# Optimization experiments

Measured on AMD Instinct MI355X. Metric: run time of the kernel, lower is better.

Reference implementation:

```python
import jax, jax.numpy as jnp
import numpy as np
import math

B, LQ, S, D = 8, 4096, 77, 1024
H, HD = 16, 64
R, ALPHA = 192, 16.0
LORA_SCALE = ALPHA / R
N_SUBJ = 32


def setup_inputs() -> dict:
    key = jax.random.key(0)
    ks = jax.random.split(key, 16)
    w = 0.02
    return {
        "hidden_states": jax.random.normal(ks[0], (B, LQ, D), jnp.float32),
        "encoder_hidden_states": jax.random.normal(ks[1], (B, S, D), jnp.float32),
        "Wq": jax.random.normal(ks[2], (D, D), jnp.float32) * w,
        "Wk": jax.random.normal(ks[3], (D, D), jnp.float32) * w,
        "Wv": jax.random.normal(ks[4], (D, D), jnp.float32) * w,
        "Wo": jax.random.normal(ks[5], (D, D), jnp.float32) * w,
        "bo": jnp.zeros((D,), jnp.float32),
        "Ak": jax.random.normal(ks[6], (R, D), jnp.float32) * w,
        "Bk": jax.random.normal(ks[7], (D, R), jnp.float32) * w,
        "Av": jax.random.normal(ks[8], (R, D), jnp.float32) * w,
        "Bv": jax.random.normal(ks[9], (D, R), jnp.float32) * w,
        "Ao": jax.random.normal(ks[10], (R, D), jnp.float32) * w,
        "Bo": jax.random.normal(ks[11], (D, R), jnp.float32) * w,
        "cross_attn_scale_factor": jnp.ones((), jnp.float32),
        "subj_b": jax.random.randint(ks[12], (N_SUBJ,), 0, B, jnp.int32),
        "subj_n": jax.random.randint(ks[13], (N_SUBJ,), 0, S, jnp.int32),
    }


def _lora(x, A, Bm):
    # peft LoRA delta: scale * (x @ A^T) @ B^T
    return LORA_SCALE * ((x @ A.T) @ Bm.T)


def reference(hidden_states, encoder_hidden_states, Wq, Wk, Wv, Wo, bo,
              Ak, Bk, Av, Bv, Ao, Bo, cross_attn_scale_factor, subj_b, subj_n):
    hs, ehs = hidden_states, encoder_hidden_states
    # q_lora_updates_query=False -> query uses the base projection only
    q = hs @ Wq.T                                  # [B, LQ, D]
    k = ehs @ Wk.T + _lora(ehs, Ak, Bk)            # [B, S, D] (to_k_lora)
    v = ehs @ Wv.T + _lora(ehs, Av, Bv)            # [B, S, D] (to_v_lora)

    q = q.reshape(B, LQ, H, HD).transpose(0, 2, 1, 3)   # [B,H,LQ,HD]
    k = k.reshape(B, S, H, HD).transpose(0, 2, 1, 3)    # [B,H,S,HD]
    v = v.reshape(B, S, H, HD).transpose(0, 2, 1, 3)

    scale = 1.0 / math.sqrt(HD)
    attn_score = jnp.einsum('bhld,bhsd->bhls', q, k) * scale  # [B,H,LQ,S]

    # normalize_cross_attn: zero-center subject-token scores over query dim,
    # then rescale by the learned cross_attn_scale_factor.
    sub = attn_score[subj_b, :, :, subj_n]                    # [K,H,LQ]
    sub = (sub - sub.mean(axis=2, keepdims=True)) * cross_attn_scale_factor
    attn_score = attn_score.at[subj_b, :, :, subj_n].set(sub)

    attn_weight = jax.nn.softmax(attn_score, axis=-1)
    out = jnp.einsum('bhls,bhsd->bhld', attn_weight, v)       # [B,H,LQ,HD]
    out = out.transpose(0, 2, 1, 3).reshape(B, LQ, D)

    # to_out_lora: base out-proj (with bias) + LoRA delta; to_out[1] dropout = id
    out = out @ Wo.T + bo + _lora(out, Ao, Bo)
    return out
```

## Files before the change

kernel.cpp:

```cpp
#include <hip/hip_runtime.h>
#include <stdint.h>

#define B_     8
#define LQ_    4096
#define S_     77
#define SP_    80
#define D_     1024
#define H_     16
#define HD_    64
#define NC_    1280
#define NSUBJ_ 32

typedef __attribute__((ext_vector_type(4))) float  f4;
typedef __attribute__((ext_vector_type(8))) short  short8;
typedef __attribute__((ext_vector_type(8))) unsigned short us8;
typedef __attribute__((ext_vector_type(4))) unsigned short us4;

__device__ __forceinline__ unsigned short f2bf(float f) {
  union { float f; unsigned u; } x; x.f = f;
  unsigned r = x.u + 0x7FFFu + ((x.u >> 16) & 1u);
  return (unsigned short)(r >> 16);
}
__device__ __forceinline__ float bf2f(unsigned short v) {
  union { unsigned u; float f; } x; x.u = ((unsigned)v) << 16;
  return x.f;
}

__device__ __forceinline__ void gload16(const void* g, void* s) {
  __builtin_amdgcn_global_load_lds((const __attribute__((address_space(1))) void*)g,
                                   (__attribute__((address_space(3))) void*)s, 16, 0, 0);
}

__global__ __launch_bounds__(256) void k_hssum(const float* __restrict__ hs,
                                               float* __restrict__ part,
                                               unsigned short* __restrict__ hsb) {
  int b = blockIdx.y;
  size_t base = ((size_t)b * LQ_ + (size_t)blockIdx.x * 64) * D_ + threadIdx.x * 4;
  f4 acc = {0.f, 0.f, 0.f, 0.f};
  for (int l = 0; l < 64; ++l) {
    f4 v = *(const f4*)(hs + base + (size_t)l * D_);
    acc += v;
    if (hsb) {
      us4 o;
#pragma unroll
      for (int j = 0; j < 4; ++j) o[j] = f2bf(v[j]);
      *(us4*)(hsb + base + (size_t)l * D_) = o;
    }
  }
  *(f4*)(part + (size_t)blockIdx.x * (B_ * D_) + b * D_ + threadIdx.x * 4) = acc;
}

__global__ __launch_bounds__(256) void k_hsred(const float* __restrict__ part,
                                               float* __restrict__ hssum) {
  int i = blockIdx.x * 256 + threadIdx.x;
  float s = 0.f;
  for (int x = 0; x < 64; ++x) s += part[(size_t)x * (B_ * D_) + i];
  hssum[i] = s;
}

__global__ __launch_bounds__(256) void k_ehsb(const float* __restrict__ ehs,
                                              unsigned short* __restrict__ ehsb) {
  int s = blockIdx.x, b = blockIdx.y;
  int i = threadIdx.x * 4;
  us4 o = {0, 0, 0, 0};
  if (s < S_) {
    f4 v = *(const f4*)(ehs + ((size_t)b * S_ + s) * D_ + i);
#pragma unroll
    for (int j = 0; j < 4; ++j) o[j] = f2bf(v[j]);
  }
  *(us4*)(ehsb + ((size_t)b * SP_ + s) * D_ + i) = o;
}

__global__ __launch_bounds__(256) void k_tr4(const float* __restrict__ Wq, const float* __restrict__ Ak,
                                             const float* __restrict__ Av, const float* __restrict__ Ao,
                                             unsigned short* __restrict__ wqTb, float* __restrict__ akT,
                                             float* __restrict__ avT, float* __restrict__ aoT) {
  int z = blockIdx.z;
  const float* in = z == 0 ? Wq : (z == 1 ? Ak : (z == 2 ? Av : Ao));
  float* outf = z == 1 ? akT : (z == 2 ? avT : aoT);
  int R = z == 0 ? 1024 : 192;
  const int C = 1024;
  int c0 = blockIdx.x * 32, r0 = blockIdx.y * 32;
  if (r0 >= R) return;
  __shared__ float tile[32][33];
  int tx = threadIdx.x & 31, ty = threadIdx.x >> 5;
#pragma unroll
  for (int k = 0; k < 4; ++k)
    tile[ty + 8 * k][tx] = in[(size_t)(r0 + ty + 8 * k) * C + c0 + tx];
  __syncthreads();
#pragma unroll
  for (int k = 0; k < 4; ++k) {
    size_t idx = (size_t)(c0 + ty + 8 * k) * R + r0 + tx;
    float v = tile[tx][ty + 8 * k];
    if (z == 0) wqTb[idx] = f2bf(v);
    else        outf[idx] = v;
  }
}

template <bool OBF>
__device__ __forceinline__ void gemm64_body(
    const float* __restrict__ A, int lda, const float* __restrict__ Bt, int ldb,
    void* __restrict__ Cv, int ldc, long cbase, const float* __restrict__ Dm, int ldd,
    int M, int Mv, int N, int K, float alpha, int m0, int n0,
    short* As, short* Bs) {
  int t = threadIdx.x, lane = t & 63, wid = t >> 6;
  int wm = wid >> 1, wn = wid & 1;
  f4 acc[2][2] = {};
  int srow = t >> 2, skc = (t & 3) * 8;
  for (int k0 = 0; k0 < K; k0 += 32) {
    __syncthreads();
    f4 a0 = {0,0,0,0}, a1 = {0,0,0,0}, b0 = {0,0,0,0}, b1 = {0,0,0,0};
    if (m0 + srow < Mv) {
      const float* p = A + (size_t)(m0 + srow) * lda + k0 + skc;
      a0 = *(const f4*)p; a1 = *(const f4*)(p + 4);
    }
    if (n0 + srow < N) {
      const float* p = Bt + (size_t)(n0 + srow) * ldb + k0 + skc;
      b0 = *(const f4*)p; b1 = *(const f4*)(p + 4);
    }
    us8 ua, ub;
#pragma unroll
    for (int j = 0; j < 4; ++j) {
      ua[j] = f2bf(a0[j]); ua[4 + j] = f2bf(a1[j]);
      ub[j] = f2bf(b0[j]); ub[4 + j] = f2bf(b1[j]);
    }
    *(us8*)(As + srow * 40 + skc) = ua;
    *(us8*)(Bs + srow * 40 + skc) = ub;
    __syncthreads();
    short8 fa[2], fb[2];
#pragma unroll
    for (int i = 0; i < 2; ++i) {
      fa[i] = *(const short8*)(As + (wm * 32 + i * 16 + (lane & 15)) * 40 + (lane >> 4) * 8);
      fb[i] = *(const short8*)(Bs + (wn * 32 + i * 16 + (lane & 15)) * 40 + (lane >> 4) * 8);
    }
#pragma unroll
    for (int mi = 0; mi < 2; ++mi)
#pragma unroll
      for (int ni = 0; ni < 2; ++ni)
        acc[mi][ni] = __builtin_amdgcn_mfma_f32_16x16x32_bf16(fa[mi], fb[ni], acc[mi][ni], 0, 0, 0);
  }
#pragma unroll
  for (int mi = 0; mi < 2; ++mi)
#pragma unroll
    for (int ni = 0; ni < 2; ++ni)
#pragma unroll
      for (int j = 0; j < 4; ++j) {
        int row = m0 + wm * 32 + mi * 16 + (lane >> 4) * 4 + j;
        int col = n0 + wn * 32 + ni * 16 + (lane & 15);
        if (row < M && col < N) {
          float val = acc[mi][ni][j] * alpha;
          if (Dm) val += Dm[(size_t)row * ldd + col];
          size_t idx = (size_t)cbase + (size_t)row * ldc + col;
          if (OBF) ((unsigned short*)Cv)[idx] = f2bf(val);
          else     ((float*)Cv)[idx] = val;
        }
      }
}

__global__ __launch_bounds__(256) void k_weff(
    const float* __restrict__ Bk, const float* __restrict__ Bv, const float* __restrict__ Bo,
    const float* __restrict__ akT, const float* __restrict__ avT, const float* __restrict__ aoT,
    const float* __restrict__ Wk, const float* __restrict__ Wv, const float* __restrict__ Wo,
    unsigned short* __restrict__ wEb, float alpha) {
  int z = blockIdx.z;
  const float* A  = z == 0 ? Bk : (z == 1 ? Bv : Bo);
  const float* Bt = z == 0 ? akT : (z == 1 ? avT : aoT);
  const float* Dm = z == 0 ? Wk : (z == 1 ? Wv : Wo);
  __shared__ short As[64 * 40];
  __shared__ short Bs[64 * 40];
  gemm64_body<true>(A, 192, Bt, 192, wEb + (size_t)z * 1048576, 1024, 0, Dm, 1024,
                    1024, 1024, 1024, 192, alpha, blockIdx.x * 64, blockIdx.y * 64, As, Bs);
}

__global__ __launch_bounds__(512) void k_kv(const unsigned short* __restrict__ ehsb,
                                            const unsigned short* __restrict__ wEb,
                                            unsigned short* __restrict__ kvb) {
  __shared__ short As[80 * 64];
  __shared__ short Bs[256 * 64];
  int b = blockIdx.x >> 3, nt = blockIdx.x & 7;
  int n0 = nt * 256;
  const unsigned short* Ab = ehsb + (size_t)b * SP_ * D_;
  int t = threadIdx.x, lane = t & 63, w = t >> 6;
  int r = lane & 15, q = lane >> 4;
  f4 acc[5][2] = {};

  for (int k0 = 0; k0 < 1024; k0 += 64) {
    __syncthreads();
#pragma unroll
    for (int p = 0; p < 6; ++p) {
      int cb = p * 512 + w * 64;
      if (cb < 2688) {
        int cc = cb + lane;
        if (cb < 640) {
          int row = cc >> 3, gc = (cc & 7) ^ (row & 7);
          gload16(Ab + (size_t)row * D_ + k0 + gc * 8, (char*)As + cb * 16);
        } else {
          int bc = cc - 640, row = bc >> 3, gc = (bc & 7) ^ (row & 7);
          gload16(wEb + (size_t)(n0 + row) * D_ + k0 + gc * 8, (char*)Bs + (cb - 640) * 16);
        }
      }
    }
    __syncthreads();
#pragma unroll
    for (int kk = 0; kk < 2; ++kk) {
      int co = ((kk * 4 + q) ^ (r & 7)) * 8;
      short8 fa[5], fb[2];
#pragma unroll
      for (int mi = 0; mi < 5; ++mi)
        fa[mi] = *(const short8*)(As + (mi * 16 + r) * 64 + co);
#pragma unroll
      for (int ni = 0; ni < 2; ++ni)
        fb[ni] = *(const short8*)(Bs + (w * 32 + ni * 16 + r) * 64 + co);
#pragma unroll
      for (int mi = 0; mi < 5; ++mi)
#pragma unroll
        for (int ni = 0; ni < 2; ++ni)
          acc[mi][ni] = __builtin_amdgcn_mfma_f32_16x16x32_bf16(fa[mi], fb[ni], acc[mi][ni], 0, 0, 0);
    }
  }
#pragma unroll
  for (int mi = 0; mi < 5; ++mi)
#pragma unroll
    for (int ni = 0; ni < 2; ++ni)
#pragma unroll
      for (int j = 0; j < 4; ++j) {
        int s = mi * 16 + q * 4 + j;
        int col = n0 + w * 32 + ni * 16 + r;
        kvb[((size_t)b * SP_ + s) * 2048 + col] = f2bf(acc[mi][ni][j]);
      }
}

__global__ __launch_bounds__(512) void k_mtut(const unsigned short* __restrict__ kvb,
                                              const unsigned short* __restrict__ wqTb,
                                              const unsigned short* __restrict__ wEb,
                                              unsigned short* __restrict__ Mt,
                                              unsigned short* __restrict__ Ut) {
  __shared__ short Ss[80 * 64];
  __shared__ short Ls[256 * 64];
  int z = blockIdx.x;
  bool mt = z < 128;
  int zz = mt ? z : z - 128;
  int b = zz >> 4, h = zz & 15;
  const unsigned short* small_src = kvb + (size_t)b * SP_ * 2048 + (mt ? h * 64 : 1024 + h * 64);
  const unsigned short* large_src = mt ? (wqTb + h * 64) : (wEb + (size_t)2048 * 1024 + h * 64);
  int t = threadIdx.x, lane = t & 63, w = t >> 6;
  int r = lane & 15, q = lane >> 4;

#pragma unroll
  for (int p = 0; p < 2; ++p) {
    int cb = p * 512 + w * 64;
    if (cb < 640) {
      int cc = cb + lane, row = cc >> 3, gc = (cc & 7) ^ (row & 7);
      gload16(small_src + (size_t)row * 2048 + gc * 8, (char*)Ss + cb * 16);
    }
  }

  for (int mc = 0; mc < 4; ++mc) {
    __syncthreads();
#pragma unroll
    for (int p = 0; p < 4; ++p) {
      int cb = p * 512 + w * 64;
      int cc = cb + lane, row = cc >> 3, gc = (cc & 7) ^ (row & 7);
      gload16(large_src + (size_t)(mc * 256 + row) * 1024 + gc * 8, (char*)Ls + cb * 16);
    }
    __syncthreads();

    if (mt) {
      f4 acc[5][2] = {};
#pragma unroll
      for (int kk = 0; kk < 2; ++kk) {
        int co = ((kk * 4 + q) ^ (r & 7)) * 8;
        short8 fa[5], fb[2];
#pragma unroll
        for (int mi = 0; mi < 5; ++mi)
          fa[mi] = *(const short8*)(Ss + (mi * 16 + r) * 64 + co);
#pragma unroll
        for (int ni = 0; ni < 2; ++ni)
          fb[ni] = *(const short8*)(Ls + (w * 32 + ni * 16 + r) * 64 + co);
#pragma unroll
        for (int mi = 0; mi < 5; ++mi)
#pragma unroll
          for (int ni = 0; ni < 2; ++ni)
            acc[mi][ni] = __builtin_amdgcn_mfma_f32_16x16x32_bf16(fa[mi], fb[ni], acc[mi][ni], 0, 0, 0);
      }
#pragma unroll
      for (int mi = 0; mi < 5; ++mi)
#pragma unroll
        for (int ni = 0; ni < 2; ++ni)
#pragma unroll
          for (int j = 0; j < 4; ++j) {
            int s = mi * 16 + q * 4 + j;
            int e = mc * 256 + w * 32 + ni * 16 + r;
            Mt[((size_t)b * NC_ + h * SP_ + s) * 1024 + e] = f2bf(acc[mi][ni][j] * 0.125f);
          }
    } else {
      f4 acc[2][5] = {};
#pragma unroll
      for (int kk = 0; kk < 2; ++kk) {
        int co = ((kk * 4 + q) ^ (r & 7)) * 8;
        short8 fa[2], fb[5];
#pragma unroll
        for (int mi = 0; mi < 2; ++mi)
          fa[mi] = *(const short8*)(Ls + (w * 32 + mi * 16 + r) * 64 + co);
#pragma unroll
        for (int ni = 0; ni < 5; ++ni)
          fb[ni] = *(const short8*)(Ss + (ni * 16 + r) * 64 + co);
#pragma unroll
        for (int mi = 0; mi < 2; ++mi)
#pragma unroll
          for (int ni = 0; ni < 5; ++ni)
            acc[mi][ni] = __builtin_amdgcn_mfma_f32_16x16x32_bf16(fa[mi], fb[ni], acc[mi][ni], 0, 0, 0);
      }
#pragma unroll
      for (int mi = 0; mi < 2; ++mi)
#pragma unroll
        for (int ni = 0; ni < 5; ++ni)
#pragma unroll
          for (int j = 0; j < 4; ++j) {
            int e = mc * 256 + w * 32 + mi * 16 + q * 4 + j;
            int col = h * SP_ + ni * 16 + r;
            Ut[((size_t)b * D_ + e) * NC_ + col] = f2bf(acc[mi][ni][j]);
          }
    }
  }
}

__global__ void k_mubeta(const float* __restrict__ hssum, const float* __restrict__ Wq,
                         const unsigned short* __restrict__ kvb,
                         const int* __restrict__ sb, const int* __restrict__ sn,
                         const float* __restrict__ csf_p,
                         float* __restrict__ alphav, float* __restrict__ betav) {
  int h = blockIdx.x, b = blockIdx.y;
  int t = threadIdx.x;
  __shared__ float qp[64];
  {
    int hd = t >> 1, half = t & 1;
    const float* wr = Wq + (size_t)(h * 64 + hd) * D_ + half * 512;
    const float* hp = hssum + b * D_ + half * 512;
    float s = 0.f;
    for (int d = 0; d < 512; d += 4) {
      f4 w = *(const f4*)(wr + d);
      f4 x = *(const f4*)(hp + d);
      s += w[0] * x[0] + w[1] * x[1] + w[2] * x[2] + w[3] * x[3];
    }
    s += __shfl_xor(s, 1, 64);
    if (half == 0) qp[hd] = s * (1.f / 4096.f);
  }
  __syncthreads();
  int s = t;
  if (s >= SP_) return;
  const unsigned short* kp = kvb + ((size_t)(b * SP_ + s)) * 2048 + h * HD_;
  float mu = 0.f;
#pragma unroll
  for (int hd = 0; hd < HD_; hd += 4) {
    us4 kv = *(const us4*)(kp + hd);
#pragma unroll
    for (int j = 0; j < 4; ++j) mu += qp[hd + j] * bf2f(kv[j]);
  }
  mu *= 0.125f;
  bool subj = false;
  for (int i = 0; i < NSUBJ_; ++i) subj = subj || (sb[i] == b && sn[i] == s);
  float csf = *csf_p;
  int c = b * NC_ + h * SP_ + s;
  alphav[c] = subj ? csf : 1.f;
  betav[c] = (s >= S_) ? -1e30f : (subj ? -mu * csf : 0.f);
}

__global__ __launch_bounds__(512, 2) void k_score_big(
    const unsigned short* __restrict__ hsb, const unsigned short* __restrict__ Mt,
    const float* __restrict__ alphav, const float* __restrict__ betav,
    unsigned short* __restrict__ P) {
  extern __shared__ short lds[];
  int id = blockIdx.x;
  int x = id & 7, idp = id >> 3;
  int nt = idp & 3;
  int pid = (idp >> 2) * 8 + x;
  int b = pid >> 4, mt = pid & 15;
  int m0 = mt * 256, n0 = nt * 320;

  const unsigned short* Ab = hsb + (size_t)b * LQ_ * D_;
  const unsigned short* Bb = Mt + (size_t)b * NC_ * D_;
  const float* alp = alphav + b * NC_;
  const float* bet = betav + b * NC_;
  unsigned short* Pb = P + (size_t)b * LQ_ * NC_;

  int t = threadIdx.x, lane = t & 63, wid = t >> 6;
  int wm = wid >> 2, wn = wid & 3;
  int r = lane & 15, q = lane >> 4;
  f4 acc[8][5] = {};

  auto SA = [&](int bf, int k0, int p) {
    int cb = p * 512 + wid * 64;
    int cc = cb + lane;
    int row = cc >> 2, gc = (cc & 3) ^ ((row >> 1) & 3);
    gload16(Ab + (size_t)(m0 + row) * D_ + k0 + gc * 8, (char*)(lds + bf * 8192) + cb * 16);
  };
  auto SB = [&](int bf, int k0, int p) {
    int cb = p * 512 + wid * 64;
    int cc = cb + lane;
    int row = cc >> 2, gc = (cc & 3) ^ ((row >> 1) & 3);
    gload16(Bb + (size_t)(n0 + row) * D_ + k0 + gc * 8, (char*)(lds + 32768 + bf * 10240) + cb * 16);
  };
  auto SBx = [&](int bf, int k0) {
    if (wid < 4) {
      int cb = 1024 + wid * 64;
      int cc = cb + lane;
      int row = cc >> 2, gc = (cc & 3) ^ ((row >> 1) & 3);
      gload16(Bb + (size_t)(n0 + row) * D_ + k0 + gc * 8, (char*)(lds + 32768 + bf * 10240) + cb * 16);
    }
  };
  auto STAGE_P1 = [&](int h) { if (h < 32) { int bf = h & 3, k0 = h * 32; SA(bf, k0, 0); SA(bf, k0, 1); SB(bf, k0, 0); } };
  auto STAGE_P2 = [&](int h) { if (h < 32) { int bf = h & 3, k0 = h * 32; SB(bf, k0, 1); SBx(bf, k0); } };

  STAGE_P1(0); STAGE_P2(0);
  STAGE_P1(1); STAGE_P2(1);
  STAGE_P1(2); STAGE_P2(2);
  if (wid < 4) asm volatile("s_waitcnt vmcnt(10)" ::: "memory");
  else         asm volatile("s_waitcnt vmcnt(8)" ::: "memory");
  __builtin_amdgcn_s_barrier();

#pragma unroll 1
  for (int h = 0; h < 32; ++h) {
    int bf = h & 3;
    const short* Ar = lds + bf * 8192;
    const short* Br = lds + 32768 + bf * 10240;
    short8 fa[4], fb[5];

#pragma unroll
    for (int ni = 0; ni < 5; ++ni) {
      int row = wn * 80 + ni * 16 + r;
      fb[ni] = *(const short8*)(Br + row * 32 + ((q ^ ((row >> 1) & 3)) * 8));
    }
#pragma unroll
    for (int mi = 0; mi < 4; ++mi) {
      int row = wm * 128 + mi * 16 + r;
      fa[mi] = *(const short8*)(Ar + row * 32 + ((q ^ ((row >> 1) & 3)) * 8));
    }
    __builtin_amdgcn_sched_barrier(0);
    STAGE_P1(h + 3);
    __builtin_amdgcn_sched_barrier(0);
    __builtin_amdgcn_s_barrier();
    asm volatile("s_waitcnt lgkmcnt(0)");
    __builtin_amdgcn_s_setprio(1);
#pragma unroll
    for (int mi = 0; mi < 4; ++mi)
#pragma unroll
      for (int ni = 0; ni < 5; ++ni)
        acc[mi][ni] = __builtin_amdgcn_mfma_f32_16x16x32_bf16(fa[mi], fb[ni], acc[mi][ni], 0, 0, 0);
    __builtin_amdgcn_s_setprio(0);

#pragma unroll
    for (int mi = 0; mi < 4; ++mi) {
      int row = wm * 128 + (4 + mi) * 16 + r;
      fa[mi] = *(const short8*)(Ar + row * 32 + ((q ^ ((row >> 1) & 3)) * 8));
    }
    __builtin_amdgcn_sched_barrier(0);
    STAGE_P2(h + 3);
    __builtin_amdgcn_sched_barrier(0);
    __builtin_amdgcn_s_barrier();
    asm volatile("s_waitcnt lgkmcnt(0)");
    __builtin_amdgcn_s_setprio(1);
#pragma unroll
    for (int mi = 0; mi < 4; ++mi)
#pragma unroll
      for (int ni = 0; ni < 5; ++ni)
        acc[4 + mi][ni] = __builtin_amdgcn_mfma_f32_16x16x32_bf16(fa[mi], fb[ni], acc[4 + mi][ni], 0, 0, 0);
    __builtin_amdgcn_s_setprio(0);

    if (h <= 28) {
      if (wid < 4) asm volatile("s_waitcnt vmcnt(10)" ::: "memory");
      else         asm volatile("s_waitcnt vmcnt(8)" ::: "memory");
    } else if (h == 29) {
      if (wid < 4) asm volatile("s_waitcnt vmcnt(5)" ::: "memory");
      else         asm volatile("s_waitcnt vmcnt(4)" ::: "memory");
    } else if (h == 30) {
      asm volatile("s_waitcnt vmcnt(0)" ::: "memory");
    }
    if (h < 31) __builtin_amdgcn_s_barrier();
  }

  float al[5], be[5];
#pragma unroll
  for (int ni = 0; ni < 5; ++ni) {
    int cc = n0 + wn * 80 + ni * 16 + r;
    al[ni] = alp[cc]; be[ni] = bet[cc];
  }
#pragma unroll
  for (int mi = 0; mi < 8; ++mi) {
#pragma unroll
    for (int j = 0; j < 4; ++j) {
      float v[5];
      float m = -3.0e38f;
#pragma unroll
      for (int ni = 0; ni < 5; ++ni) { v[ni] = acc[mi][ni][j] * al[ni] + be[ni]; m = fmaxf(m, v[ni]); }
#pragma unroll
      for (int off = 1; off < 16; off <<= 1) m = fmaxf(m, __shfl_xor(m, off, 64));
      float ssum = 0.f;
#pragma unroll
      for (int ni = 0; ni < 5; ++ni) { v[ni] = __expf(v[ni] - m); ssum += v[ni]; }
#pragma unroll
      for (int off = 1; off < 16; off <<= 1) ssum += __shfl_xor(ssum, off, 64);
      float inv = 1.f / ssum;
      int row = m0 + wm * 128 + mi * 16 + q * 4 + j;
      size_t rb = (size_t)row * NC_ + n0 + wn * 80 + r;
#pragma unroll
      for (int ni = 0; ni < 5; ++ni)
        Pb[rb + ni * 16] = f2bf(v[ni] * inv);
    }
  }
}

__global__ __launch_bounds__(256) void k_score_f32(
    const float* __restrict__ hs, const unsigned short* __restrict__ Mt,
    const float* __restrict__ alphav, const float* __restrict__ betav,
    unsigned short* __restrict__ P) {
  int id = blockIdx.x;
  int x = id & 7, idp = id >> 3;
  int n_t = idp & 7;
  int pid = (idp >> 3) * 8 + x;
  int b = pid >> 5, m_t = pid & 31;
  int m0 = m_t * 128, n0 = n_t * 160;
  const float* Af = hs + (size_t)b * LQ_ * D_;
  const unsigned short* Bb = Mt + (size_t)b * NC_ * D_;
  const float* alp = alphav + b * NC_;
  const float* bet = betav + b * NC_;
  unsigned short* Pb = P + (size_t)b * LQ_ * NC_;
  __shared__ short As[128 * 64];
  __shared__ short Bs[160 * 64];
  int t = threadIdx.x, lane = t & 63, wid = t >> 6;
  int wm = wid >> 1, wn = wid & 1;
  int srow = lane >> 3;
  int schunk = (lane & 7) ^ srow;
  f4 acc[4][5] = {};
  for (int k0 = 0; k0 < D_; k0 += 64) {
    __syncthreads();
    for (int i = wid; i < 20; i += 4)
      gload16(Bb + (size_t)(n0 + i * 8 + srow) * D_ + k0 + schunk * 8, (char*)Bs + i * 1024);
    int arow = t >> 3, ac = t & 7;
    int awc = ac ^ (arow & 7);
#pragma unroll
    for (int p = 0; p < 4; ++p) {
      int row = p * 32 + arow;
      const float* src = Af + (size_t)(m0 + row) * D_ + k0 + ac * 8;
      f4 v0 = *(const f4*)src;
      f4 v1 = *(const f4*)(src + 4);
      us8 u;
#pragma unroll
      for (int j = 0; j < 4; ++j) { u[j] = f2bf(v0[j]); u[4 + j] = f2bf(v1[j]); }
      *(us8*)(As + row * 64 + awc * 8) = u;
    }
    __syncthreads();
#pragma unroll
    for (int kk = 0; kk < 2; ++kk) {
      int co = ((kk * 4 + (lane >> 4)) ^ (lane & 7)) * 8;
      short8 fa[4], fb[5];
#pragma unroll
      for (int mi = 0; mi < 4; ++mi)
        fa[mi] = *(const short8*)(As + (wm * 64 + mi * 16 + (lane & 15)) * 64 + co);
#pragma unroll
      for (int ni = 0; ni < 5; ++ni)
        fb[ni] = *(const short8*)(Bs + (wn * 80 + ni * 16 + (lane & 15)) * 64 + co);
#pragma unroll
      for (int mi = 0; mi < 4; ++mi)
#pragma unroll
        for (int ni = 0; ni < 5; ++ni)
          acc[mi][ni] = __builtin_amdgcn_mfma_f32_16x16x32_bf16(fa[mi], fb[ni], acc[mi][ni], 0, 0, 0);
    }
  }
  float al[5], be[5];
#pragma unroll
  for (int ni = 0; ni < 5; ++ni) {
    int cc = n0 + wn * 80 + ni * 16 + (lane & 15);
    al[ni] = alp[cc]; be[ni] = bet[cc];
  }
#pragma unroll
  for (int mi = 0; mi < 4; ++mi) {
#pragma unroll
    for (int j = 0; j < 4; ++j) {
      float v[5];
      float m = -3.0e38f;
#pragma unroll
      for (int ni = 0; ni < 5; ++ni) { v[ni] = acc[mi][ni][j] * al[ni] + be[ni]; m = fmaxf(m, v[ni]); }
#pragma unroll
      for (int off = 1; off < 16; off <<= 1) m = fmaxf(m, __shfl_xor(m, off, 64));
      float ssum = 0.f;
#pragma unroll
      for (int ni = 0; ni < 5; ++ni) { v[ni] = __expf(v[ni] - m); ssum += v[ni]; }
#pragma unroll
      for (int off = 1; off < 16; off <<= 1) ssum += __shfl_xor(ssum, off, 64);
      float inv = 1.f / ssum;
      int row = m0 + wm * 64 + mi * 16 + (lane >> 4) * 4 + j;
      size_t rb = (size_t)row * NC_ + n0 + wn * 80 + (lane & 15);
#pragma unroll
      for (int ni = 0; ni < 5; ++ni)
        Pb[rb + ni * 16] = f2bf(v[ni] * inv);
    }
  }
}

__global__ __launch_bounds__(512, 2) void k_out_big(
    const unsigned short* __restrict__ P, const unsigned short* __restrict__ Ut,
    const float* __restrict__ bo, float* __restrict__ out) {
  extern __shared__ short lds[];
  int id = blockIdx.x;
  int x = id & 7, idp = id >> 3;
  int nt = idp & 3;
  int pid = (idp >> 2) * 8 + x;
  int b = pid >> 4, mt = pid & 15;
  int m0 = mt * 256, n0 = nt * 256;

  const unsigned short* Ab = P + (size_t)b * LQ_ * NC_;
  const unsigned short* Bb = Ut + (size_t)b * D_ * NC_;
  float* ob = out + (size_t)b * LQ_ * D_;

  int t = threadIdx.x, lane = t & 63, wid = t >> 6;
  int wm = wid >> 2, wn = wid & 3;
  int r = lane & 15, q = lane >> 4;
  f4 acc[8][4] = {};
  const int T = NC_ / 32;

  auto SA = [&](int bf, int k0, int p) {
    int cb = p * 512 + wid * 64;
    int cc = cb + lane;
    int row = cc >> 2, gc = (cc & 3) ^ ((row >> 1) & 3);
    gload16(Ab + (size_t)(m0 + row) * NC_ + k0 + gc * 8, (char*)(lds + bf * 8192) + cb * 16);
  };
  auto SB = [&](int bf, int k0, int p) {
    int cb = p * 512 + wid * 64;
    int cc = cb + lane;
    int row = cc >> 2, gc = (cc & 3) ^ ((row >> 1) & 3);
    gload16(Bb + (size_t)(n0 + row) * NC_ + k0 + gc * 8, (char*)(lds + 32768 + bf * 8192) + cb * 16);
  };
  auto STAGE_P1 = [&](int h) { if (h < T) { int bf = h & 3, k0 = h * 32; SA(bf, k0, 0); SA(bf, k0, 1); } };
  auto STAGE_P2 = [&](int h) { if (h < T) { int bf = h & 3, k0 = h * 32; SB(bf, k0, 0); SB(bf, k0, 1); } };

  STAGE_P1(0); STAGE_P2(0);
  STAGE_P1(1); STAGE_P2(1);
  STAGE_P1(2); STAGE_P2(2);
  asm volatile("s_waitcnt vmcnt(8)" ::: "memory");
  __builtin_amdgcn_s_barrier();

#pragma unroll 1
  for (int h = 0; h < T; ++h) {
    int bf = h & 3;
    const short* Ar = lds + bf * 8192;
    const short* Br = lds + 32768 + bf * 8192;
    short8 fa[4], fb[4];

#pragma unroll
    for (int ni = 0; ni < 4; ++ni) {
      int row = wn * 64 + ni * 16 + r;
      fb[ni] = *(const short8*)(Br + row * 32 + ((q ^ ((row >> 1) & 3)) * 8));
    }
#pragma unroll
    for (int mi = 0; mi < 4; ++mi) {
      int row = wm * 128 + mi * 16 + r;
      fa[mi] = *(const short8*)(Ar + row * 32 + ((q ^ ((row >> 1) & 3)) * 8));
    }
    __builtin_amdgcn_sched_barrier(0);
    STAGE_P1(h + 3);
    __builtin_amdgcn_sched_barrier(0);
    __builtin_amdgcn_s_barrier();
    asm volatile("s_waitcnt lgkmcnt(0)");
    __builtin_amdgcn_s_setprio(1);
#pragma unroll
    for (int mi = 0; mi < 4; ++mi)
#pragma unroll
      for (int ni = 0; ni < 4; ++ni)
        acc[mi][ni] = __builtin_amdgcn_mfma_f32_16x16x32_bf16(fa[mi], fb[ni], acc[mi][ni], 0, 0, 0);
    __builtin_amdgcn_s_setprio(0);

#pragma unroll
    for (int mi = 0; mi < 4; ++mi) {
      int row = wm * 128 + (4 + mi) * 16 + r;
      fa[mi] = *(const short8*)(Ar + row * 32 + ((q ^ ((row >> 1) & 3)) * 8));
    }
    __builtin_amdgcn_sched_barrier(0);
    STAGE_P2(h + 3);
    __builtin_amdgcn_sched_barrier(0);
    __builtin_amdgcn_s_barrier();
    asm volatile("s_waitcnt lgkmcnt(0)");
    __builtin_amdgcn_s_setprio(1);
#pragma unroll
    for (int mi = 0; mi < 4; ++mi)
#pragma unroll
      for (int ni = 0; ni < 4; ++ni)
        acc[4 + mi][ni] = __builtin_amdgcn_mfma_f32_16x16x32_bf16(fa[mi], fb[ni], acc[4 + mi][ni], 0, 0, 0);
    __builtin_amdgcn_s_setprio(0);

    if (h <= T - 4) {
      asm volatile("s_waitcnt vmcnt(8)" ::: "memory");
    } else if (h == T - 3) {
      asm volatile("s_waitcnt vmcnt(4)" ::: "memory");
    } else if (h == T - 2) {
      asm volatile("s_waitcnt vmcnt(0)" ::: "memory");
    }
    if (h < T - 1) __builtin_amdgcn_s_barrier();
  }

#pragma unroll
  for (int ni = 0; ni < 4; ++ni) {
    int col = n0 + wn * 64 + ni * 16 + r;
    float bov = bo[col];
#pragma unroll
    for (int mi = 0; mi < 8; ++mi)
#pragma unroll
      for (int j = 0; j < 4; ++j) {
        int row = m0 + wm * 128 + mi * 16 + q * 4 + j;
        ob[(size_t)row * D_ + col] = acc[mi][ni][j] + bov;
      }
  }
}

extern "C" void kernel_launch(void* const* d_in, const int* in_sizes, int n_in,
                              void* d_out, int out_size, void* d_ws, size_t ws_size,
                              hipStream_t stream) {
  const float* hs  = (const float*)d_in[0];
  const float* ehs = (const float*)d_in[1];
  const float* Wq  = (const float*)d_in[2];
  const float* Wk  = (const float*)d_in[3];
  const float* Wv  = (const float*)d_in[4];
  const float* Wo  = (const float*)d_in[5];
  const float* bo  = (const float*)d_in[6];
  const float* Ak  = (const float*)d_in[7];
  const float* Bk  = (const float*)d_in[8];
  const float* Av  = (const float*)d_in[9];
  const float* Bv  = (const float*)d_in[10];
  const float* Ao  = (const float*)d_in[11];
  const float* Bo  = (const float*)d_in[12];
  const float* csf = (const float*)d_in[13];
  const int*   sb  = (const int*)d_in[14];
  const int*   sn  = (const int*)d_in[15];
  float* out = (float*)d_out;

  hipFuncSetAttribute(reinterpret_cast<const void*>(k_score_big),
                      hipFuncAttributeMaxDynamicSharedMemorySize, 147456);
  hipFuncSetAttribute(reinterpret_cast<const void*>(k_out_big),
                      hipFuncAttributeMaxDynamicSharedMemorySize, 131072);

  char* ws = (char*)d_ws;
  unsigned short* P  = (unsigned short*)ws;
  unsigned short* Mt = (unsigned short*)(ws + 83886080);
  unsigned short* Ut = (unsigned short*)(ws + 104857600);
  const size_t NEED_HSB = 125829120ULL + 67108864ULL + 81920ULL;
  bool useHsb = ws_size >= NEED_HSB;
  unsigned short* hsb = useHsb ? (unsigned short*)(ws + 125829120) : nullptr;
  char* tail = useHsb ? (ws + 192937984) : (ws + 125829120);
  float* alphav = (float*)tail;
  float* betav  = (float*)(tail + 40960);
  unsigned short* kvb   = (unsigned short*)(ws + 0);
  unsigned short* wEb   = (unsigned short*)(ws + 2621440);
  unsigned short* wqTb  = (unsigned short*)(ws + 8912896);
  float*          aT    = (float*)(ws + 11010048);
  unsigned short* ehsb  = (unsigned short*)(ws + 13369344);
  float*          part  = (float*)(ws + 14680064);
  float*          hssum = (float*)(ws + 16777216);

  float* akT = aT;
  float* avT = aT + 196608;
  float* aoT = aT + 393216;

  const float LS = 16.0f / 192.0f;

  k_hssum<<<dim3(64, 8), 256, 0, stream>>>(hs, part, hsb);
  k_hsred<<<32, 256, 0, stream>>>(part, hssum);

  k_tr4<<<dim3(32, 32, 4), 256, 0, stream>>>(Wq, Ak, Av, Ao, wqTb, akT, avT, aoT);
  k_ehsb<<<dim3(SP_, B_), 256, 0, stream>>>(ehs, ehsb);

  k_weff<<<dim3(16, 16, 3), 256, 0, stream>>>(Bk, Bv, Bo, akT, avT, aoT, Wk, Wv, Wo, wEb, LS);

  k_kv<<<64, 512, 0, stream>>>(ehsb, wEb, kvb);

  k_mtut<<<256, 512, 0, stream>>>(kvb, wqTb, wEb, Mt, Ut);

  k_mubeta<<<dim3(16, 8), 128, 0, stream>>>(hssum, Wq, kvb, sb, sn, csf, alphav, betav);

  if (useHsb)
    k_score_big<<<512, 512, 147456, stream>>>(hsb, Mt, alphav, betav, P);
  else
    k_score_f32<<<2048, 256, 0, stream>>>(hs, Mt, alphav, betav, P);
  k_out_big<<<512, 512, 131072, stream>>>(P, Ut, bo, out);

  (void)in_sizes; (void)n_in; (void)out_size; (void)ws_size;
}
```

Measured before the change: 344.2 us.

## Merge prep kernels, pre-convert LoRA factors to bf16, retile weight-merge and KV GEMMs

Folds the transpose, ehs conversion and new B-factor bf16 conversion into one prep launch, so the weight-merge GEMM reads bf16 operands through async 16-byte loads into swizzled LDS. The merge GEMM moves from 64x64 to 128x128 tiles with a larger K step. The KV projection GEMM splits into 256 smaller blocks of 64 columns for more parallelism. These are small preprocessing kernels next to the large score and output kernels, so the overall effect is probably minor.

```diff
diff --git a/kernel.cpp b/kernel.cpp
--- a/kernel.cpp
+++ b/kernel.cpp
@@ -58,138 +58,140 @@
   hssum[i] = s;
 }
 
-__global__ __launch_bounds__(256) void k_ehsb(const float* __restrict__ ehs,
-                                              unsigned short* __restrict__ ehsb) {
-  int s = blockIdx.x, b = blockIdx.y;
-  int i = threadIdx.x * 4;
-  us4 o = {0, 0, 0, 0};
-  if (s < S_) {
-    f4 v = *(const f4*)(ehs + ((size_t)b * S_ + s) * D_ + i);
+__global__ __launch_bounds__(256) void k_prep(
+    const float* __restrict__ Wq, const float* __restrict__ Ak,
+    const float* __restrict__ Av, const float* __restrict__ Ao,
+    const float* __restrict__ ehs,
+    const float* __restrict__ Bk, const float* __restrict__ Bv, const float* __restrict__ Bo,
+    unsigned short* __restrict__ wqTb, unsigned short* __restrict__ aTb,
+    unsigned short* __restrict__ ehsb, unsigned short* __restrict__ bxb) {
+  int z = blockIdx.z;
+  int t = threadIdx.x;
+  if (z == 4) {
+    if (blockIdx.y >= 20) return;
+    int gr = blockIdx.y * 32 + (t >> 3);
+    int col = blockIdx.x * 32 + (t & 7) * 4;
+    int b = gr / SP_, s = gr - b * SP_;
+    us4 o = {0, 0, 0, 0};
+    if (s < S_) {
+      f4 v = *(const f4*)(ehs + ((size_t)b * S_ + s) * D_ + col);
+#pragma unroll
+      for (int j = 0; j < 4; ++j) o[j] = f2bf(v[j]);
+    }
+    *(us4*)(ehsb + (size_t)gr * D_ + col) = o;
+    return;
+  }
+  if (z >= 5) {
+    if (blockIdx.x >= 6) return;
+    const float* in = z == 5 ? Bk : (z == 6 ? Bv : Bo);
+    unsigned short* outp = bxb + (size_t)(z - 5) * 1024 * 192;
+    int rr = blockIdx.y * 32 + (t >> 3);
+    int c = blockIdx.x * 32 + (t & 7) * 4;
+    f4 v = *(const f4*)(in + (size_t)rr * 192 + c);
+    us4 o;
 #pragma unroll
     for (int j = 0; j < 4; ++j) o[j] = f2bf(v[j]);
-  }
-  *(us4*)(ehsb + ((size_t)b * SP_ + s) * D_ + i) = o;
-}
-
-__global__ __launch_bounds__(256) void k_tr4(const float* __restrict__ Wq, const float* __restrict__ Ak,
-                                             const float* __restrict__ Av, const float* __restrict__ Ao,
-                                             unsigned short* __restrict__ wqTb, float* __restrict__ akT,
-                                             float* __restrict__ avT, float* __restrict__ aoT) {
-  int z = blockIdx.z;
+    *(us4*)(outp + (size_t)rr * 192 + c) = o;
+    return;
+  }
   const float* in = z == 0 ? Wq : (z == 1 ? Ak : (z == 2 ? Av : Ao));
-  float* outf = z == 1 ? akT : (z == 2 ? avT : aoT);
   int R = z == 0 ? 1024 : 192;
-  const int C = 1024;
   int c0 = blockIdx.x * 32, r0 = blockIdx.y * 32;
   if (r0 >= R) return;
   __shared__ float tile[32][33];
-  int tx = threadIdx.x & 31, ty = threadIdx.x >> 5;
+  int tx = t & 31, ty = t >> 5;
 #pragma unroll
   for (int k = 0; k < 4; ++k)
-    tile[ty + 8 * k][tx] = in[(size_t)(r0 + ty + 8 * k) * C + c0 + tx];
+    tile[ty + 8 * k][tx] = in[(size_t)(r0 + ty + 8 * k) * 1024 + c0 + tx];
   __syncthreads();
-#pragma unroll
-  for (int k = 0; k < 4; ++k) {
-    size_t idx = (size_t)(c0 + ty + 8 * k) * R + r0 + tx;
-    float v = tile[tx][ty + 8 * k];
-    if (z == 0) wqTb[idx] = f2bf(v);
-    else        outf[idx] = v;
-  }
-}
-
-template <bool OBF>
-__device__ __forceinline__ void gemm64_body(
-    const float* __restrict__ A, int lda, const float* __restrict__ Bt, int ldb,
-    void* __restrict__ Cv, int ldc, long cbase, const float* __restrict__ Dm, int ldd,
-    int M, int Mv, int N, int K, float alpha, int m0, int n0,
-    short* As, short* Bs) {
-  int t = threadIdx.x, lane = t & 63, wid = t >> 6;
-  int wm = wid >> 1, wn = wid & 1;
-  f4 acc[2][2] = {};
-  int srow = t >> 2, skc = (t & 3) * 8;
-  for (int k0 = 0; k0 < K; k0 += 32) {
-    __syncthreads();
-    f4 a0 = {0,0,0,0}, a1 = {0,0,0,0}, b0 = {0,0,0,0}, b1 = {0,0,0,0};
-    if (m0 + srow < Mv) {
-      const float* p = A + (size_t)(m0 + srow) * lda + k0 + skc;
-      a0 = *(const f4*)p; a1 = *(const f4*)(p + 4);
-    }
-    if (n0 + srow < N) {
-      const float* p = Bt + (size_t)(n0 + srow) * ldb + k0 + skc;
-      b0 = *(const f4*)p; b1 = *(const f4*)(p + 4);
-    }
-    us8 ua, ub;
-#pragma unroll
-    for (int j = 0; j < 4; ++j) {
-      ua[j] = f2bf(a0[j]); ua[4 + j] = f2bf(a1[j]);
-      ub[j] = f2bf(b0[j]); ub[4 + j] = f2bf(b1[j]);
-    }
-    *(us8*)(As + srow * 40 + skc) = ua;
-    *(us8*)(Bs + srow * 40 + skc) = ub;
-    __syncthreads();
-    short8 fa[2], fb[2];
-#pragma unroll
-    for (int i = 0; i < 2; ++i) {
-      fa[i] = *(const short8*)(As + (wm * 32 + i * 16 + (lane & 15)) * 40 + (lane >> 4) * 8);
-      fb[i] = *(const short8*)(Bs + (wn * 32 + i * 16 + (lane & 15)) * 40 + (lane >> 4) * 8);
-    }
-#pragma unroll
-    for (int mi = 0; mi < 2; ++mi)
-#pragma unroll
-      for (int ni = 0; ni < 2; ++ni)
-        acc[mi][ni] = __builtin_amdgcn_mfma_f32_16x16x32_bf16(fa[mi], fb[ni], acc[mi][ni], 0, 0, 0);
-  }
-#pragma unroll
-  for (int mi = 0; mi < 2; ++mi)
-#pragma unroll
-    for (int ni = 0; ni < 2; ++ni)
-#pragma unroll
-      for (int j = 0; j < 4; ++j) {
-        int row = m0 + wm * 32 + mi * 16 + (lane >> 4) * 4 + j;
-        int col = n0 + wn * 32 + ni * 16 + (lane & 15);
-        if (row < M && col < N) {
-          float val = acc[mi][ni][j] * alpha;
-          if (Dm) val += Dm[(size_t)row * ldd + col];
-          size_t idx = (size_t)cbase + (size_t)row * ldc + col;
-          if (OBF) ((unsigned short*)Cv)[idx] = f2bf(val);
-          else     ((float*)Cv)[idx] = val;
-        }
-      }
-}
-
-__global__ __launch_bounds__(256) void k_weff(
-    const float* __restrict__ Bk, const float* __restrict__ Bv, const float* __restrict__ Bo,
-    const float* __restrict__ akT, const float* __restrict__ avT, const float* __restrict__ aoT,
+  unsigned short* outp = z == 0 ? wqTb : (aTb + (size_t)(z - 1) * 1024 * 192);
+#pragma unroll
+  for (int k = 0; k < 4; ++k)
+    outp[(size_t)(c0 + ty + 8 * k) * R + r0 + tx] = f2bf(tile[tx][ty + 8 * k]);
+}
+
+__global__ __launch_bounds__(256) void k_weff_big(
+    const unsigned short* __restrict__ bxb, const unsigned short* __restrict__ aTb,
     const float* __restrict__ Wk, const float* __restrict__ Wv, const float* __restrict__ Wo,
     unsigned short* __restrict__ wEb, float alpha) {
+  __shared__ short As[128 * 64];
+  __shared__ short Bs[128 * 64];
   int z = blockIdx.z;
-  const float* A  = z == 0 ? Bk : (z == 1 ? Bv : Bo);
-  const float* Bt = z == 0 ? akT : (z == 1 ? avT : aoT);
+  const unsigned short* Ab = bxb + (size_t)z * 1024 * 192;
+  const unsigned short* Bb = aTb + (size_t)z * 1024 * 192;
   const float* Dm = z == 0 ? Wk : (z == 1 ? Wv : Wo);
-  __shared__ short As[64 * 40];
-  __shared__ short Bs[64 * 40];
-  gemm64_body<true>(A, 192, Bt, 192, wEb + (size_t)z * 1048576, 1024, 0, Dm, 1024,
-                    1024, 1024, 1024, 192, alpha, blockIdx.x * 64, blockIdx.y * 64, As, Bs);
-}
-
-__global__ __launch_bounds__(512) void k_kv(const unsigned short* __restrict__ ehsb,
+  int m0 = blockIdx.x * 128, n0 = blockIdx.y * 128;
+  int t = threadIdx.x, lane = t & 63, w = t >> 6;
+  int wm = w >> 1, wn = w & 1;
+  int r = lane & 15, q = lane >> 4;
+  f4 acc[4][4] = {};
+
+  for (int k0 = 0; k0 < 192; k0 += 64) {
+    __syncthreads();
+#pragma unroll
+    for (int p = 0; p < 8; ++p) {
+      int cb = p * 256 + w * 64;
+      int cc = cb + lane;
+      if (cb < 1024) {
+        int row = cc >> 3, gc = (cc & 7) ^ (row & 7);
+        gload16(Ab + (size_t)(m0 + row) * 192 + k0 + gc * 8, (char*)As + cb * 16);
+      } else {
+        int bc = cc - 1024, row = bc >> 3, gc = (bc & 7) ^ (row & 7);
+        gload16(Bb + (size_t)(n0 + row) * 192 + k0 + gc * 8, (char*)Bs + (cb - 1024) * 16);
+      }
+    }
+    __syncthreads();
+#pragma unroll
+    for (int kk = 0; kk < 2; ++kk) {
+      short8 fa[4], fb[4];
+#pragma unroll
+      for (int mi = 0; mi < 4; ++mi) {
+        int row = wm * 64 + mi * 16 + r;
+        fa[mi] = *(const short8*)(As + row * 64 + (((kk * 4 + q) ^ (row & 7)) * 8));
+      }
+#pragma unroll
+      for (int ni = 0; ni < 4; ++ni) {
+        int row = wn * 64 + ni * 16 + r;
+        fb[ni] = *(const short8*)(Bs + row * 64 + (((kk * 4 + q) ^ (row & 7)) * 8));
+      }
+#pragma unroll
+      for (int mi = 0; mi < 4; ++mi)
+#pragma unroll
+        for (int ni = 0; ni < 4; ++ni)
+          acc[mi][ni] = __builtin_amdgcn_mfma_f32_16x16x32_bf16(fa[mi], fb[ni], acc[mi][ni], 0, 0, 0);
+    }
+  }
+#pragma unroll
+  for (int mi = 0; mi < 4; ++mi)
+#pragma unroll
+    for (int ni = 0; ni < 4; ++ni)
+#pragma unroll
+      for (int j = 0; j < 4; ++j) {
+        int row = m0 + wm * 64 + mi * 16 + q * 4 + j;
+        int col = n0 + wn * 64 + ni * 16 + r;
+        float val = acc[mi][ni][j] * alpha + Dm[(size_t)row * 1024 + col];
+        wEb[(size_t)z * 1048576 + (size_t)row * 1024 + col] = f2bf(val);
+      }
+}
+
+__global__ __launch_bounds__(256) void k_kv(const unsigned short* __restrict__ ehsb,
                                             const unsigned short* __restrict__ wEb,
                                             unsigned short* __restrict__ kvb) {
   __shared__ short As[80 * 64];
-  __shared__ short Bs[256 * 64];
-  int b = blockIdx.x >> 3, nt = blockIdx.x & 7;
-  int n0 = nt * 256;
+  __shared__ short Bs[64 * 64];
+  int b = blockIdx.x >> 5, nt = blockIdx.x & 31;
+  int n0 = nt * 64;
   const unsigned short* Ab = ehsb + (size_t)b * SP_ * D_;
   int t = threadIdx.x, lane = t & 63, w = t >> 6;
   int r = lane & 15, q = lane >> 4;
-  f4 acc[5][2] = {};
+  f4 acc[5] = {{0,0,0,0},{0,0,0,0},{0,0,0,0},{0,0,0,0},{0,0,0,0}};
 
   for (int k0 = 0; k0 < 1024; k0 += 64) {
     __syncthreads();
 #pragma unroll
-    for (int p = 0; p < 6; ++p) {
-      int cb = p * 512 + w * 64;
-      if (cb < 2688) {
+    for (int p = 0; p < 5; ++p) {
+      int cb = p * 256 + w * 64;
+      if (cb < 1152) {
         int cc = cb + lane;
         if (cb < 640) {
           int row = cc >> 3, gc = (cc & 7) ^ (row & 7);
@@ -203,31 +205,29 @@
     __syncthreads();
 #pragma unroll
     for (int kk = 0; kk < 2; ++kk) {
-      int co = ((kk * 4 + q) ^ (r & 7)) * 8;
-      short8 fa[5], fb[2];
+      short8 fa[5], fb;
+      {
+        int row = w * 16 + r;
+        fb = *(const short8*)(Bs + row * 64 + (((kk * 4 + q) ^ (row & 7)) * 8));
+      }
+#pragma unroll
+      for (int mi = 0; mi < 5; ++mi) {
+        int row = mi * 16 + r;
+        fa[mi] = *(const short8*)(As + row * 64 + (((kk * 4 + q) ^ (row & 7)) * 8));
+      }
 #pragma unroll
       for (int mi = 0; mi < 5; ++mi)
-        fa[mi] = *(const short8*)(As + (mi * 16 + r) * 64 + co);
-#pragma unroll
-      for (int ni = 0; ni < 2; ++ni)
-        fb[ni] = *(const short8*)(Bs + (w * 32 + ni * 16 + r) * 64 + co);
-#pragma unroll
-      for (int mi = 0; mi < 5; ++mi)
-#pragma unroll
-        for (int ni = 0; ni < 2; ++ni)
-          acc[mi][ni] = __builtin_amdgcn_mfma_f32_16x16x32_bf16(fa[mi], fb[ni], acc[mi][ni], 0, 0, 0);
+        acc[mi] = __builtin_amdgcn_mfma_f32_16x16x32_bf16(fa[mi], fb, acc[mi], 0, 0, 0);
     }
   }
 #pragma unroll
   for (int mi = 0; mi < 5; ++mi)
 #pragma unroll
-    for (int ni = 0; ni < 2; ++ni)
-#pragma unroll
-      for (int j = 0; j < 4; ++j) {
-        int s = mi * 16 + q * 4 + j;
-        int col = n0 + w * 32 + ni * 16 + r;
-        kvb[((size_t)b * SP_ + s) * 2048 + col] = f2bf(acc[mi][ni][j]);
-      }
+    for (int j = 0; j < 4; ++j) {
+      int s = mi * 16 + q * 4 + j;
+      int col = n0 + w * 16 + r;
+      kvb[((size_t)b * SP_ + s) * 2048 + col] = f2bf(acc[mi][j]);
+    }
 }
 
 __global__ __launch_bounds__(512) void k_mtut(const unsigned short* __restrict__ kvb,
@@ -751,26 +751,23 @@
   unsigned short* kvb   = (unsigned short*)(ws + 0);
   unsigned short* wEb   = (unsigned short*)(ws + 2621440);
   unsigned short* wqTb  = (unsigned short*)(ws + 8912896);
-  float*          aT    = (float*)(ws + 11010048);
+  unsigned short* aTb   = (unsigned short*)(ws + 11010048);
+  unsigned short* bxb   = (unsigned short*)(ws + 12189696);
   unsigned short* ehsb  = (unsigned short*)(ws + 13369344);
   float*          part  = (float*)(ws + 14680064);
   float*          hssum = (float*)(ws + 16777216);
 
-  float* akT = aT;
-  float* avT = aT + 196608;
-  float* aoT = aT + 393216;
-
   const float LS = 16.0f / 192.0f;
 
   k_hssum<<<dim3(64, 8), 256, 0, stream>>>(hs, part, hsb);
   k_hsred<<<32, 256, 0, stream>>>(part, hssum);
 
-  k_tr4<<<dim3(32, 32, 4), 256, 0, stream>>>(Wq, Ak, Av, Ao, wqTb, akT, avT, aoT);
-  k_ehsb<<<dim3(SP_, B_), 256, 0, stream>>>(ehs, ehsb);
-
-  k_weff<<<dim3(16, 16, 3), 256, 0, stream>>>(Bk, Bv, Bo, akT, avT, aoT, Wk, Wv, Wo, wEb, LS);
-
-  k_kv<<<64, 512, 0, stream>>>(ehsb, wEb, kvb);
+  k_prep<<<dim3(32, 32, 8), 256, 0, stream>>>(Wq, Ak, Av, Ao, ehs, Bk, Bv, Bo,
+                                              wqTb, aTb, ehsb, bxb);
+
+  k_weff_big<<<dim3(8, 8, 3), 256, 0, stream>>>(bxb, aTb, Wk, Wv, Wo, wEb, LS);
+
+  k_kv<<<256, 256, 0, stream>>>(ehsb, wEb, kvb);
 
   k_mtut<<<256, 512, 0, stream>>>(kvb, wqTb, wEb, Mt, Ut);
 
```

After: 331.1 us. 1.04x faster.
